# Performance work log

Hardware: AMD Instinct MI355X
Metric: run time of the kernel (lower is better)

The kernel has to match this reference:

```python
import jax, jax.numpy as jnp
import numpy as np

DIM = 512
HEADS = 8
R = 8  # reduction_ratio
EPS = 1e-08


def setup_inputs() -> dict:
    key = jax.random.key(0)
    k1, k2, k3, k4, k5 = jax.random.split(key, 5)
    B, H, W = 2, 128, 128
    x = jax.random.normal(k1, (B, DIM, H, W), dtype=jnp.float32)
    mask = jax.random.uniform(k2, (B, 1, H, W), dtype=jnp.float32)
    # learned params (conv weights, OIHW)
    Wq = jax.random.normal(k3, (DIM, DIM, 1, 1), dtype=jnp.float32) * 0.02
    Wkv = jax.random.normal(k4, (2 * DIM, DIM, R, R), dtype=jnp.float32) * 0.02
    Wo = jax.random.normal(k5, (DIM, DIM, 1, 1), dtype=jnp.float32) * 0.02
    return {"x": x, "mask": mask, "Wq": Wq, "Wkv": Wkv, "Wo": Wo}


def reference(x, mask, Wq, Wkv, Wo):
    B, C, H, W = x.shape
    heads = HEADS
    hd = C // heads  # head dim
    scale = hd ** (-0.5)
    N = H * W
    Hr, Wr = H // R, W // R
    L = Hr * Wr

    # to_q: 1x1 conv (no bias)
    q = jnp.einsum('bchw,oc->bohw', x, Wq[:, :, 0, 0])
    # to_kv: conv kernel R stride R (no bias)
    kv = jax.lax.conv_general_dilated(
        x, Wkv, window_strides=(R, R), padding='VALID',
        dimension_numbers=('NCHW', 'OIHW', 'NCHW'))
    k, v = jnp.split(kv, 2, axis=1)  # each [B, C, Hr, Wr]

    # nn.Unfold(R, stride=R) on [B,1,H,W] then mean over patch dim == avg-pool R/R
    mask_down = mask.reshape(B, Hr, R, Wr, R).mean(axis=(2, 4)).reshape(B, L)  # [B, L]
    m_flat = mask.reshape(B, N)  # [B, N]  (c == 1)
    # rank-1 outer-product bias, then log
    bias = jnp.log(m_flat[:, :, None] * mask_down[:, None, :] + EPS)  # [B, N, L]

    def to_tokens(t, n):
        # 'b (h c) x y -> (b h) (x y) c'
        Bt = t.shape[0]
        return t.reshape(Bt, heads, hd, n).transpose(0, 1, 3, 2).reshape(Bt * heads, n, hd)

    qh = to_tokens(q, N)   # [B*heads, N, hd]
    kh = to_tokens(k, L)   # [B*heads, L, hd]
    vh = to_tokens(v, L)   # [B*heads, L, hd]

    # torch mask.repeat(heads,1,1): tiles whole [B,...] block heads times -> index i uses bias[i % B]
    bias_rep = jnp.tile(bias, (heads, 1, 1))  # [heads*B, N, L]

    sim = (jnp.einsum('bic,bjc->bij', qh, kh) + bias_rep) * scale
    attn = jax.nn.softmax(sim, axis=-1)
    out = jnp.einsum('bij,bjc->bic', attn, vh)  # [B*heads, N, hd]

    # '(b h) (x y) c -> b (h c) x y'
    out = out.reshape(B, heads, N, hd).transpose(0, 1, 3, 2).reshape(B, C, H, W)
    return jnp.einsum('bchw,oc->bohw', out, Wo[:, :, 0, 0])
```

## Files before the change

kernel.cpp:

```cpp
#include <hip/hip_runtime.h>
#include <math.h>

#define DIMC  512
#define HEADS 8
#define HD    64
#define NPIX  16384
#define LTOK  256
#define BATCH 2
#define WIMG  128
#define KVK   32768
#define EPSB  1e-8f
#define SCALEF 0.125f
#define SPLITK 16
#define KCHUNK (KVK / SPLITK)

typedef unsigned short ushort_t;
typedef unsigned int uint_t;
using bf16x8 = __attribute__((ext_vector_type(8))) __bf16;
using f32x4  = __attribute__((ext_vector_type(4))) float;

__device__ __forceinline__ ushort_t f2bf(float f) {
    union { float f; unsigned u; } v; v.f = f;
    unsigned r = v.u + 0x7FFFu + ((v.u >> 16) & 1u);
    return (ushort_t)(r >> 16);
}
__device__ __forceinline__ uint_t pk2bf(float a, float b) {
    return (uint_t)f2bf(a) | ((uint_t)f2bf(b) << 16);
}
__device__ __forceinline__ void gl16(const void* g, void* l) {
    __builtin_amdgcn_global_load_lds(
        (const __attribute__((address_space(1))) unsigned int*)g,
        (__attribute__((address_space(3))) unsigned int*)l, 16, 0, 0);
}

__global__ void k_maskdown(const float* __restrict__ mask, float* __restrict__ md) {
    int b = blockIdx.x;
    int l = threadIdx.x;
    int hr = l >> 4, wr = l & 15;
    const float* mp = mask + (size_t)b * NPIX;
    float s = 0.f;
#pragma unroll
    for (int i = 0; i < 8; ++i)
#pragma unroll
        for (int j = 0; j < 8; ++j)
            s += mp[(hr * 8 + i) * WIMG + wr * 8 + j];
    md[b * LTOK + l] = s * (1.f / 64.f);
}

__global__ __launch_bounds__(256) void k_xt(const float* __restrict__ x, ushort_t* __restrict__ xt) {
    __shared__ float t[64][65];
    int b = blockIdx.z, c0 = blockIdx.y * 64, n0 = blockIdx.x * 64;
    int tn = threadIdx.x & 63, tc = threadIdx.x >> 6;
    const float* xb = x + ((size_t)b * DIMC + c0) * NPIX + n0;
#pragma unroll
    for (int p = 0; p < 16; ++p)
        t[tc + p * 4][tn] = xb[(size_t)(tc + p * 4) * NPIX + tn];
    __syncthreads();
    ushort_t* xtb = xt + ((size_t)b * NPIX + n0) * DIMC + c0;
    int tc4 = threadIdx.x & 15, ng = threadIdx.x >> 4;
#pragma unroll
    for (int p = 0; p < 4; ++p) {
        int nl = ng + p * 16;
        ushort4 v;
        v.x = f2bf(t[4 * tc4 + 0][nl]);
        v.y = f2bf(t[4 * tc4 + 1][nl]);
        v.z = f2bf(t[4 * tc4 + 2][nl]);
        v.w = f2bf(t[4 * tc4 + 3][nl]);
        *(ushort4*)&xtb[(size_t)nl * DIMC + 4 * tc4] = v;
    }
}

__global__ __launch_bounds__(256) void k_wkvp(const float* __restrict__ Wkv, ushort_t* __restrict__ Wp) {
    __shared__ float t[64][65];
    int o = blockIdx.y, c0 = blockIdx.x * 64;
    int tij = threadIdx.x & 63, tc = threadIdx.x >> 6;
    const float* wb = Wkv + ((size_t)o * DIMC + c0) * 64;
#pragma unroll
    for (int p = 0; p < 16; ++p)
        t[tc + p * 4][tij] = wb[(size_t)(tc + p * 4) * 64 + tij];
    __syncthreads();
    ushort_t* wpb = Wp + (size_t)o * KVK + c0;
    int tj4 = threadIdx.x & 15, ig = threadIdx.x >> 4;
#pragma unroll
    for (int p = 0; p < 4; ++p) {
        int ij = ig + p * 16;
        ushort4 v;
        v.x = f2bf(t[4 * tj4 + 0][ij]);
        v.y = f2bf(t[4 * tj4 + 1][ij]);
        v.z = f2bf(t[4 * tj4 + 2][ij]);
        v.w = f2bf(t[4 * tj4 + 3][ij]);
        *(ushort4*)&wpb[(size_t)ij * DIMC + 4 * tj4] = v;
    }
}

__global__ void k_cvt2(const float* __restrict__ a, const float* __restrict__ b,
                       ushort_t* __restrict__ da, ushort_t* __restrict__ db) {
    int i = blockIdx.x * 256 + threadIdx.x;
    if (i < 262144) da[i] = f2bf(a[i]);
    else            db[i - 262144] = f2bf(b[i - 262144]);
}

template<int EPI>
__global__ __launch_bounds__(256) void k_gemm_qo(
    const ushort_t* __restrict__ A, long sA,
    const ushort_t* __restrict__ B, long sB,
    void* __restrict__ Yv) {
    __shared__ ushort_t Asm[2][128 * 64];
    __shared__ ushort_t Bsm[2][128 * 64];
    const int tid = threadIdx.x;
    const int w = tid >> 6, lane = tid & 63;
    const int wm = w >> 1, wn = w & 1;
    const int lr = lane & 15, lg = lane >> 4;
    const int bz = blockIdx.z;
    const int m0 = blockIdx.y * 128, c0 = blockIdx.x * 128;
    const ushort_t* Ab = A + (size_t)bz * sA;
    const ushort_t* Bb = B + (size_t)bz * sB;

    f32x4 acc[4][4];
    const f32x4 zz = {0.f, 0.f, 0.f, 0.f};
#pragma unroll
    for (int i = 0; i < 4; ++i)
#pragma unroll
        for (int j = 0; j < 4; ++j) acc[i][j] = zz;

#define STAGE_QO(buf, k0) do {                                               \
    _Pragma("unroll")                                                        \
    for (int r = 0; r < 4; ++r) {                                            \
        int slot = r * 256 + tid;                                            \
        int m = slot >> 3, kb = slot & 7;                                    \
        int kbs = kb ^ (m & 7);                                              \
        gl16(Ab + (size_t)(m0 + m) * DIMC + (k0) + kbs * 8,                  \
             &Asm[buf][(size_t)(r * 256 + w * 64) * 8]);                     \
    }                                                                        \
    _Pragma("unroll")                                                        \
    for (int r = 0; r < 4; ++r) {                                            \
        int slot = r * 256 + tid;                                            \
        int m = slot >> 3, kb = slot & 7;                                    \
        int kbs = kb ^ (m & 7);                                              \
        gl16(Bb + (size_t)(c0 + m) * DIMC + (k0) + kbs * 8,                  \
             &Bsm[buf][(size_t)(r * 256 + w * 64) * 8]);                     \
    }                                                                        \
} while (0)

    STAGE_QO(0, 0);
    __syncthreads();
    int cur = 0;
#pragma unroll 1
    for (int t = 0; t < 8; ++t) {
        if (t < 7) STAGE_QO(cur ^ 1, (t + 1) * 64);
#pragma unroll
        for (int kk = 0; kk < 2; ++kk) {
            bf16x8 af[4], bfr[4];
#pragma unroll
            for (int i = 0; i < 4; ++i) {
                int row = wm * 64 + i * 16 + lr;
                af[i] = *(const bf16x8*)&Asm[cur][(size_t)(row * 8 + ((kk * 4 + lg) ^ (row & 7))) * 8];
            }
#pragma unroll
            for (int j = 0; j < 4; ++j) {
                int row = wn * 64 + j * 16 + lr;
                bfr[j] = *(const bf16x8*)&Bsm[cur][(size_t)(row * 8 + ((kk * 4 + lg) ^ (row & 7))) * 8];
            }
#pragma unroll
            for (int i = 0; i < 4; ++i)
#pragma unroll
                for (int j = 0; j < 4; ++j)
                    acc[i][j] = __builtin_amdgcn_mfma_f32_16x16x32_bf16(af[i], bfr[j], acc[i][j], 0, 0, 0);
        }
        if (t < 7) {
            __syncthreads();
            cur ^= 1;
        }
    }
#undef STAGE_QO

    if (EPI == 0) {
        ushort_t* q = (ushort_t*)Yv + (size_t)bz * ((size_t)NPIX * DIMC);
#pragma unroll
        for (int i = 0; i < 4; ++i) {
            int d0 = m0 + wm * 64 + i * 16 + lg * 4;
#pragma unroll
            for (int j = 0; j < 4; ++j) {
                int n = c0 + wn * 64 + j * 16 + lr;
                ushort4 v;
                v.x = f2bf(acc[i][j][0]); v.y = f2bf(acc[i][j][1]);
                v.z = f2bf(acc[i][j][2]); v.w = f2bf(acc[i][j][3]);
                *(ushort4*)&q[(size_t)n * DIMC + d0] = v;
            }
        }
    } else {
        float* O = (float*)Yv + (size_t)bz * ((size_t)DIMC * NPIX);
#pragma unroll
        for (int i = 0; i < 4; ++i) {
            int n0r = m0 + wm * 64 + i * 16 + lg * 4;
#pragma unroll
            for (int j = 0; j < 4; ++j) {
                int o = c0 + wn * 64 + j * 16 + lr;
                *(f32x4*)&O[(size_t)o * NPIX + n0r] = acc[i][j];
            }
        }
    }
}

__global__ __launch_bounds__(256) void k_convkv_mfma(
    const ushort_t* __restrict__ xt, const ushort_t* __restrict__ Wp,
    float* __restrict__ part) {
    __shared__ ushort_t Asm[2][128 * 64];
    __shared__ ushort_t Bsm[2][128 * 64];
    const int tid = threadIdx.x;
    const int w = tid >> 6, lane = tid & 63;
    const int wm = w >> 1, wn = w & 1;
    const int lr = lane & 15, lg = lane >> 4;
    const int f = blockIdx.x;
    const int xcd = f & 7, idx = f >> 3;
    const int z = (idx >> 4) * 8 + xcd;
    const int inner = idx & 15;
    const int m0 = (inner >> 1) * 128, n0 = (inner & 1) * 128;
    const int b = z >> 4, ks = z & 15;
    const ushort_t* xtb = xt + (size_t)b * NPIX * DIMC;
    const int kbeg = ks * KCHUNK;

    f32x4 acc[4][4];
    const f32x4 zz = {0.f, 0.f, 0.f, 0.f};
#pragma unroll
    for (int i = 0; i < 4; ++i)
#pragma unroll
        for (int j = 0; j < 4; ++j) acc[i][j] = zz;

#define STAGE_KV(buf, k0) do {                                               \
    _Pragma("unroll")                                                        \
    for (int r = 0; r < 4; ++r) {                                            \
        int slot = r * 256 + tid;                                            \
        int m = slot >> 3, kb = slot & 7;                                    \
        int kbs = kb ^ (m & 7);                                              \
        gl16(Wp + (size_t)(m0 + m) * KVK + (k0) + kbs * 8,                   \
             &Asm[buf][(size_t)(r * 256 + w * 64) * 8]);                     \
    }                                                                        \
    _Pragma("unroll")                                                        \
    for (int r = 0; r < 4; ++r) {                                            \
        int slot = r * 256 + tid;                                            \
        int nn = slot >> 3, kb = slot & 7;                                   \
        int l = n0 + nn, hr = l >> 4, wr = l & 15;                           \
        int kp = (k0) + (kb ^ (nn & 7)) * 8;                                 \
        int ij = kp >> 9, ck = kp & 511;                                     \
        int ii = ij >> 3, jj = ij & 7;                                       \
        gl16(xtb + (size_t)((hr * 8 + ii) * WIMG + wr * 8 + jj) * DIMC + ck, \
             &Bsm[buf][(size_t)(r * 256 + w * 64) * 8]);                     \
    }                                                                        \
} while (0)

    STAGE_KV(0, kbeg);
    __syncthreads();
    int cur = 0;
#pragma unroll 1
    for (int t = 0; t < KCHUNK / 64; ++t) {
        if (t < KCHUNK / 64 - 1) STAGE_KV(cur ^ 1, kbeg + (t + 1) * 64);
#pragma unroll
        for (int kk = 0; kk < 2; ++kk) {
            bf16x8 af[4], bfr[4];
#pragma unroll
            for (int i = 0; i < 4; ++i) {
                int row = wm * 64 + i * 16 + lr;
                af[i] = *(const bf16x8*)&Asm[cur][(size_t)(row * 8 + ((kk * 4 + lg) ^ (row & 7))) * 8];
            }
#pragma unroll
            for (int j = 0; j < 4; ++j) {
                int row = wn * 64 + j * 16 + lr;
                bfr[j] = *(const bf16x8*)&Bsm[cur][(size_t)(row * 8 + ((kk * 4 + lg) ^ (row & 7))) * 8];
            }
#pragma unroll
            for (int i = 0; i < 4; ++i)
#pragma unroll
                for (int j = 0; j < 4; ++j)
                    acc[i][j] = __builtin_amdgcn_mfma_f32_16x16x32_bf16(af[i], bfr[j], acc[i][j], 0, 0, 0);
        }
        if (t < KCHUNK / 64 - 1) {
            __syncthreads();
            cur ^= 1;
        }
    }
#undef STAGE_KV

    float* P = part + (size_t)z * (LTOK * 1024);
#pragma unroll
    for (int i = 0; i < 4; ++i) {
        int o0 = m0 + wm * 64 + i * 16 + lg * 4;
#pragma unroll
        for (int j = 0; j < 4; ++j) {
            int l = n0 + wn * 64 + j * 16 + lr;
            *(f32x4*)&P[(size_t)l * 1024 + o0] = acc[i][j];
        }
    }
}

__global__ void k_kvreduce(const float* __restrict__ part,
                           ushort_t* __restrict__ kt, ushort_t* __restrict__ vt) {
    int idx = blockIdx.x * 256 + threadIdx.x;
    int o = idx & 1023;
    int rest = idx >> 10;
    int l = rest & 255, b = rest >> 8;
    float s = 0.f;
#pragma unroll
    for (int ks = 0; ks < SPLITK; ++ks)
        s += part[(size_t)(b * SPLITK + ks) * (LTOK * 1024) + (size_t)l * 1024 + o];
    int h = (o >> 6) & 7, d = o & 63;
    if (o < 512)
        kt[(((size_t)b * 8 + h) * 256 + l) * 64 + d] = f2bf(s);
    else
        vt[(((size_t)b * 8 + h) * 64 + d) * 256 + l] = f2bf(s);
}

__global__ __launch_bounds__(256, 2) void k_attn_mfma(
    const ushort_t* __restrict__ qbf, const ushort_t* __restrict__ kt,
    const ushort_t* __restrict__ vt, const float* __restrict__ mask,
    const float* __restrict__ md, ushort_t* __restrict__ obuf) {
    __shared__ ushort_t Qs[128 * 64];
    __shared__ ushort_t Ks[256 * 64];
    __shared__ ushort_t Vs[64 * 256];

    const int tid = threadIdx.x;
    const int w = tid >> 6, lane = tid & 63;
    const int g = lane >> 4, ln = lane & 15;
    const int bh = blockIdx.y, b = bh >> 3, h = bh & 7;
    const int bb = bh & 1;
    const int n0 = blockIdx.x * 128;

    {
        const ushort_t* src = qbf + ((size_t)b * NPIX + n0) * DIMC + h * 64;
#pragma unroll
        for (int p = 0; p < 4; ++p) {
            int id = p * 256 + tid;
            int r = id >> 3, s = id & 7;
            uint4 v = *(const uint4*)(src + (size_t)r * DIMC + s * 8);
            *(uint4*)&Qs[(r * 8 + (s ^ (r & 7))) * 8] = v;
        }
    }
    {
        const ushort_t* src = kt + (size_t)bh * 256 * 64;
#pragma unroll
        for (int p = 0; p < 8; ++p) {
            int id = p * 256 + tid;
            int r = id >> 3, s = id & 7;
            uint4 v = *(const uint4*)(src + r * 64 + s * 8);
            *(uint4*)&Ks[(r * 8 + (s ^ (r & 7))) * 8] = v;
        }
    }
    {
        const ushort_t* src = vt + (size_t)bh * 64 * 256;
#pragma unroll
        for (int p = 0; p < 8; ++p) {
            int id = p * 256 + tid;
            int r = id >> 5, s = id & 31;
            uint4 v = *(const uint4*)(src + r * 256 + s * 8);
            *(uint4*)&Vs[(r * 32 + (s ^ (r & 7))) * 8] = v;
        }
    }
    __syncthreads();

    f32x4 acc[2][16];
    const f32x4 zz = {0.f, 0.f, 0.f, 0.f};
#pragma unroll
    for (int nf = 0; nf < 2; ++nf)
#pragma unroll
        for (int f = 0; f < 16; ++f) acc[nf][f] = zz;

    bf16x8 qf[2][2];
#pragma unroll
    for (int nf = 0; nf < 2; ++nf)
#pragma unroll
        for (int kk = 0; kk < 2; ++kk) {
            int nl = 32 * w + nf * 16 + ln;
            qf[nf][kk] = *(const bf16x8*)&Qs[(nl * 8 + ((kk * 4 + g) ^ (nl & 7))) * 8];
        }
#pragma unroll
    for (int f = 0; f < 16; ++f) {
#pragma unroll
        for (int kk = 0; kk < 2; ++kk) {
            int l = f * 16 + ln;
            bf16x8 kf = *(const bf16x8*)&Ks[(l * 8 + ((kk * 4 + g) ^ (l & 7))) * 8];
            acc[0][f] = __builtin_amdgcn_mfma_f32_16x16x32_bf16(kf, qf[0][kk], acc[0][f], 0, 0, 0);
            acc[1][f] = __builtin_amdgcn_mfma_f32_16x16x32_bf16(kf, qf[1][kk], acc[1][f], 0, 0, 0);
        }
    }

    float inv[2];
    uint2 pb[2][16];
#pragma unroll
    for (int nf = 0; nf < 2; ++nf) {
        float mval = mask[(size_t)bb * NPIX + n0 + 32 * w + nf * 16 + ln];
        float mx = -1e30f;
#pragma unroll
        for (int f = 0; f < 16; ++f) {
            float4 md4 = *(const float4*)&md[bb * LTOK + f * 16 + g * 4];
            float s0 = (acc[nf][f][0] + __logf(mval * md4.x + EPSB)) * SCALEF;
            float s1 = (acc[nf][f][1] + __logf(mval * md4.y + EPSB)) * SCALEF;
            float s2 = (acc[nf][f][2] + __logf(mval * md4.z + EPSB)) * SCALEF;
            float s3 = (acc[nf][f][3] + __logf(mval * md4.w + EPSB)) * SCALEF;
            acc[nf][f][0] = s0; acc[nf][f][1] = s1;
            acc[nf][f][2] = s2; acc[nf][f][3] = s3;
            mx = fmaxf(mx, fmaxf(fmaxf(s0, s1), fmaxf(s2, s3)));
        }
        mx = fmaxf(mx, __shfl_xor(mx, 16));
        mx = fmaxf(mx, __shfl_xor(mx, 32));
        float sum = 0.f;
#pragma unroll
        for (int f = 0; f < 16; ++f) {
            float p0 = __expf(acc[nf][f][0] - mx);
            float p1 = __expf(acc[nf][f][1] - mx);
            float p2 = __expf(acc[nf][f][2] - mx);
            float p3 = __expf(acc[nf][f][3] - mx);
            sum += (p0 + p1) + (p2 + p3);
            pb[nf][f].x = pk2bf(p0, p1);
            pb[nf][f].y = pk2bf(p2, p3);
        }
        sum += __shfl_xor(sum, 16);
        sum += __shfl_xor(sum, 32);
        inv[nf] = 1.f / sum;
    }

    f32x4 acc2[2][4];
#pragma unroll
    for (int nf = 0; nf < 2; ++nf)
#pragma unroll
        for (int df = 0; df < 4; ++df) acc2[nf][df] = zz;

    const int srcLo = ((g & 1) << 5) + ln;
    const bool selHi = (g >> 1);
#pragma unroll
    for (int ks = 0; ks < 8; ++ks) {
        bf16x8 vf[4];
#pragma unroll
        for (int df = 0; df < 4; ++df) {
            int d = df * 16 + ln;
            vf[df] = *(const bf16x8*)&Vs[(d * 32 + ((ks * 4 + g) ^ (d & 7))) * 8];
        }
#pragma unroll
        for (int nf = 0; nf < 2; ++nf) {
            uint_t e0 = pb[nf][2 * ks].x,     e1 = pb[nf][2 * ks].y;
            uint_t o0 = pb[nf][2 * ks + 1].x, o1 = pb[nf][2 * ks + 1].y;
            uint_t lo0 = __shfl((int)e0, srcLo), lo1 = __shfl((int)e1, srcLo);
            uint_t lo0b = __shfl((int)o0, srcLo), lo1b = __shfl((int)o1, srcLo);
            uint_t hi0 = __shfl((int)e0, srcLo + 16), hi1 = __shfl((int)e1, srcLo + 16);
            uint_t hi0b = __shfl((int)o0, srcLo + 16), hi1b = __shfl((int)o1, srcLo + 16);
            union { uint_t u[4]; bf16x8 v; } bfr;
            bfr.u[0] = selHi ? lo0b : lo0;
            bfr.u[1] = selHi ? lo1b : lo1;
            bfr.u[2] = selHi ? hi0b : hi0;
            bfr.u[3] = selHi ? hi1b : hi1;
#pragma unroll
            for (int df = 0; df < 4; ++df)
                acc2[nf][df] = __builtin_amdgcn_mfma_f32_16x16x32_bf16(vf[df], bfr.v, acc2[nf][df], 0, 0, 0);
        }
    }

#pragma unroll
    for (int nf = 0; nf < 2; ++nf) {
        int n = n0 + 32 * w + nf * 16 + ln;
        ushort_t* op = obuf + ((size_t)b * NPIX + n) * DIMC + h * 64;
#pragma unroll
        for (int df = 0; df < 4; ++df) {
            ushort4 v;
            v.x = f2bf(acc2[nf][df][0] * inv[nf]);
            v.y = f2bf(acc2[nf][df][1] * inv[nf]);
            v.z = f2bf(acc2[nf][df][2] * inv[nf]);
            v.w = f2bf(acc2[nf][df][3] * inv[nf]);
            *(ushort4*)&op[df * 16 + g * 4] = v;
        }
    }
}

extern "C" void kernel_launch(void* const* d_in, const int* in_sizes, int n_in,
                              void* d_out, int out_size, void* d_ws, size_t ws_size,
                              hipStream_t stream) {
    const float* x    = (const float*)d_in[0];
    const float* mask = (const float*)d_in[1];
    const float* Wq   = (const float*)d_in[2];
    const float* Wkv  = (const float*)d_in[3];
    const float* Wo   = (const float*)d_in[4];
    float* out = (float*)d_out;

    char* ws = (char*)d_ws;
    float*    md   = (float*)(ws);
    ushort_t* xt   = (ushort_t*)(ws + 4096);
    ushort_t* wkvp = (ushort_t*)(ws + 33558528);
    ushort_t* qbf  = wkvp;
    ushort_t* ktb  = (ushort_t*)(ws + 100667392);
    ushort_t* vtb  = ktb + 524288;
    ushort_t* wqb  = (ushort_t*)(ws + 102764544);
    ushort_t* wob  = wqb + 262144;
    float*    part = (float*)(ws + 103813120);
    ushort_t* aob  = (ushort_t*)part;

    k_maskdown<<<dim3(BATCH), dim3(256), 0, stream>>>(mask, md);
    k_xt<<<dim3(NPIX / 64, DIMC / 64, BATCH), dim3(256), 0, stream>>>(x, xt);
    k_cvt2<<<dim3(2048), dim3(256), 0, stream>>>(Wq, Wo, wqb, wob);
    k_wkvp<<<dim3(DIMC / 64, 1024), dim3(256), 0, stream>>>(Wkv, wkvp);

    k_convkv_mfma<<<dim3(512), dim3(256), 0, stream>>>(xt, wkvp, part);
    k_kvreduce<<<dim3(2048), dim3(256), 0, stream>>>(part, ktb, vtb);

    k_gemm_qo<0><<<dim3(NPIX / 128, DIMC / 128, BATCH), dim3(256), 0, stream>>>(
        wqb, 0L, xt, (long)NPIX * DIMC, qbf);

    k_attn_mfma<<<dim3(NPIX / 128, BATCH * HEADS), dim3(256), 0, stream>>>(
        qbf, ktb, vtb, mask, md, aob);

    k_gemm_qo<1><<<dim3(DIMC / 128, NPIX / 128, BATCH), dim3(256), 0, stream>>>(
        aob, (long)NPIX * DIMC, wob, 0L, out);
}
```

Before: 255.3 us.

## Fuse Wkv repack and bf16 conversion into conv-KV GEMM loads

Drops the separate Wkv permute/convert kernel and makes the strided KV conv GEMM read fp32 x and Wkv directly, converting to bf16 in registers before writing swizzled LDS. The K ordering changes to channel-major (c, i, j), so the weights need no permutation. Staging now goes through registers with a single LDS buffer and an extra barrier instead of direct-to-LDS double buffering. This removes a full pass over the 64MB Wkv tensor and its bf16 copy, at the cost of doubled fp32 global reads inside the GEMM and less overlap.

```diff
diff --git a/kernel.cpp b/kernel.cpp
--- a/kernel.cpp
+++ b/kernel.cpp
@@ -67,29 +67,6 @@
         v.z = f2bf(t[4 * tc4 + 2][nl]);
         v.w = f2bf(t[4 * tc4 + 3][nl]);
         *(ushort4*)&xtb[(size_t)nl * DIMC + 4 * tc4] = v;
-    }
-}
-
-__global__ __launch_bounds__(256) void k_wkvp(const float* __restrict__ Wkv, ushort_t* __restrict__ Wp) {
-    __shared__ float t[64][65];
-    int o = blockIdx.y, c0 = blockIdx.x * 64;
-    int tij = threadIdx.x & 63, tc = threadIdx.x >> 6;
-    const float* wb = Wkv + ((size_t)o * DIMC + c0) * 64;
-#pragma unroll
-    for (int p = 0; p < 16; ++p)
-        t[tc + p * 4][tij] = wb[(size_t)(tc + p * 4) * 64 + tij];
-    __syncthreads();
-    ushort_t* wpb = Wp + (size_t)o * KVK + c0;
-    int tj4 = threadIdx.x & 15, ig = threadIdx.x >> 4;
-#pragma unroll
-    for (int p = 0; p < 4; ++p) {
-        int ij = ig + p * 16;
-        ushort4 v;
-        v.x = f2bf(t[4 * tj4 + 0][ij]);
-        v.y = f2bf(t[4 * tj4 + 1][ij]);
-        v.z = f2bf(t[4 * tj4 + 2][ij]);
-        v.w = f2bf(t[4 * tj4 + 3][ij]);
-        *(ushort4*)&wpb[(size_t)ij * DIMC + 4 * tj4] = v;
     }
 }
 
@@ -203,10 +180,10 @@
 }
 
 __global__ __launch_bounds__(256) void k_convkv_mfma(
-    const ushort_t* __restrict__ xt, const ushort_t* __restrict__ Wp,
+    const float* __restrict__ x, const float* __restrict__ Wkv,
     float* __restrict__ part) {
-    __shared__ ushort_t Asm[2][128 * 64];
-    __shared__ ushort_t Bsm[2][128 * 64];
+    __shared__ ushort_t Asm[128 * 64];
+    __shared__ ushort_t Bsm[128 * 64];
     const int tid = threadIdx.x;
     const int w = tid >> 6, lane = tid & 63;
     const int wm = w >> 1, wn = w & 1;
@@ -217,9 +194,10 @@
     const int inner = idx & 15;
     const int m0 = (inner >> 1) * 128, n0 = (inner & 1) * 128;
     const int b = z >> 4, ks = z & 15;
-    const ushort_t* xtb = xt + (size_t)b * NPIX * DIMC;
+    const float* xb = x + (size_t)b * DIMC * NPIX;
     const int kbeg = ks * KCHUNK;
 
+    const int srow = tid >> 3, skb = tid & 7;
     f32x4 acc[4][4];
     const f32x4 zz = {0.f, 0.f, 0.f, 0.f};
 #pragma unroll
@@ -227,46 +205,60 @@
 #pragma unroll
         for (int j = 0; j < 4; ++j) acc[i][j] = zz;
 
-#define STAGE_KV(buf, k0) do {                                               \
+    float4 ra[4][2], rb[4][2];
+
+#define LOAD_KV(k0) do {                                                     \
     _Pragma("unroll")                                                        \
     for (int r = 0; r < 4; ++r) {                                            \
-        int slot = r * 256 + tid;                                            \
-        int m = slot >> 3, kb = slot & 7;                                    \
-        int kbs = kb ^ (m & 7);                                              \
-        gl16(Wp + (size_t)(m0 + m) * KVK + (k0) + kbs * 8,                   \
-             &Asm[buf][(size_t)(r * 256 + w * 64) * 8]);                     \
+        int m = srow + 32 * r;                                               \
+        const float* pa = Wkv + (size_t)(m0 + m) * KVK + (k0) + skb * 8;     \
+        ra[r][0] = *(const float4*)pa;                                       \
+        ra[r][1] = *(const float4*)(pa + 4);                                 \
+        int l = n0 + m, hr = l >> 4, wr = l & 15;                            \
+        const float* pb = xb + (size_t)((k0) >> 6) * NPIX                    \
+                          + (hr * 8 + skb) * WIMG + wr * 8;                  \
+        rb[r][0] = *(const float4*)pb;                                       \
+        rb[r][1] = *(const float4*)(pb + 4);                                 \
     }                                                                        \
+} while (0)
+
+#define WRITE_KV() do {                                                      \
     _Pragma("unroll")                                                        \
     for (int r = 0; r < 4; ++r) {                                            \
-        int slot = r * 256 + tid;                                            \
-        int nn = slot >> 3, kb = slot & 7;                                   \
-        int l = n0 + nn, hr = l >> 4, wr = l & 15;                           \
-        int kp = (k0) + (kb ^ (nn & 7)) * 8;                                 \
-        int ij = kp >> 9, ck = kp & 511;                                     \
-        int ii = ij >> 3, jj = ij & 7;                                       \
-        gl16(xtb + (size_t)((hr * 8 + ii) * WIMG + wr * 8 + jj) * DIMC + ck, \
-             &Bsm[buf][(size_t)(r * 256 + w * 64) * 8]);                     \
+        int m = srow + 32 * r;                                               \
+        int off = (m * 8 + (skb ^ (m & 7))) * 8;                             \
+        uint4 va, vb;                                                        \
+        va.x = pk2bf(ra[r][0].x, ra[r][0].y);                                \
+        va.y = pk2bf(ra[r][0].z, ra[r][0].w);                                \
+        va.z = pk2bf(ra[r][1].x, ra[r][1].y);                                \
+        va.w = pk2bf(ra[r][1].z, ra[r][1].w);                                \
+        vb.x = pk2bf(rb[r][0].x, rb[r][0].y);                                \
+        vb.y = pk2bf(rb[r][0].z, rb[r][0].w);                                \
+        vb.z = pk2bf(rb[r][1].x, rb[r][1].y);                                \
+        vb.w = pk2bf(rb[r][1].z, rb[r][1].w);                                \
+        *(uint4*)&Asm[off] = va;                                             \
+        *(uint4*)&Bsm[off] = vb;                                             \
     }                                                                        \
 } while (0)
 
-    STAGE_KV(0, kbeg);
+    LOAD_KV(kbeg);
+    WRITE_KV();
     __syncthreads();
-    int cur = 0;
 #pragma unroll 1
     for (int t = 0; t < KCHUNK / 64; ++t) {
-        if (t < KCHUNK / 64 - 1) STAGE_KV(cur ^ 1, kbeg + (t + 1) * 64);
+        if (t < KCHUNK / 64 - 1) LOAD_KV(kbeg + (t + 1) * 64);
 #pragma unroll
         for (int kk = 0; kk < 2; ++kk) {
             bf16x8 af[4], bfr[4];
 #pragma unroll
             for (int i = 0; i < 4; ++i) {
                 int row = wm * 64 + i * 16 + lr;
-                af[i] = *(const bf16x8*)&Asm[cur][(size_t)(row * 8 + ((kk * 4 + lg) ^ (row & 7))) * 8];
+                af[i] = *(const bf16x8*)&Asm[(size_t)(row * 8 + ((kk * 4 + lg) ^ (row & 7))) * 8];
             }
 #pragma unroll
             for (int j = 0; j < 4; ++j) {
                 int row = wn * 64 + j * 16 + lr;
-                bfr[j] = *(const bf16x8*)&Bsm[cur][(size_t)(row * 8 + ((kk * 4 + lg) ^ (row & 7))) * 8];
+                bfr[j] = *(const bf16x8*)&Bsm[(size_t)(row * 8 + ((kk * 4 + lg) ^ (row & 7))) * 8];
             }
 #pragma unroll
             for (int i = 0; i < 4; ++i)
@@ -274,12 +266,14 @@
                 for (int j = 0; j < 4; ++j)
                     acc[i][j] = __builtin_amdgcn_mfma_f32_16x16x32_bf16(af[i], bfr[j], acc[i][j], 0, 0, 0);
         }
+        __syncthreads();
         if (t < KCHUNK / 64 - 1) {
+            WRITE_KV();
             __syncthreads();
-            cur ^= 1;
-        }
-    }
-#undef STAGE_KV
+        }
+    }
+#undef LOAD_KV
+#undef WRITE_KV
 
     float* P = part + (size_t)z * (LTOK * 1024);
 #pragma unroll
@@ -482,8 +476,7 @@
     char* ws = (char*)d_ws;
     float*    md   = (float*)(ws);
     ushort_t* xt   = (ushort_t*)(ws + 4096);
-    ushort_t* wkvp = (ushort_t*)(ws + 33558528);
-    ushort_t* qbf  = wkvp;
+    ushort_t* qbf  = (ushort_t*)(ws + 33558528);
     ushort_t* ktb  = (ushort_t*)(ws + 100667392);
     ushort_t* vtb  = ktb + 524288;
     ushort_t* wqb  = (ushort_t*)(ws + 102764544);
@@ -492,11 +485,9 @@
     ushort_t* aob  = (ushort_t*)part;
 
     k_maskdown<<<dim3(BATCH), dim3(256), 0, stream>>>(mask, md);
+    k_cvt2<<<dim3(2048), dim3(256), 0, stream>>>(Wq, Wo, wqb, wob);
+    k_convkv_mfma<<<dim3(512), dim3(256), 0, stream>>>(x, Wkv, part);
     k_xt<<<dim3(NPIX / 64, DIMC / 64, BATCH), dim3(256), 0, stream>>>(x, xt);
-    k_cvt2<<<dim3(2048), dim3(256), 0, stream>>>(Wq, Wo, wqb, wob);
-    k_wkvp<<<dim3(DIMC / 64, 1024), dim3(256), 0, stream>>>(Wkv, wkvp);
-
-    k_convkv_mfma<<<dim3(512), dim3(256), 0, stream>>>(xt, wkvp, part);
     k_kvreduce<<<dim3(2048), dim3(256), 0, stream>>>(part, ktb, vtb);
 
     k_gemm_qo<0><<<dim3(NPIX / 128, DIMC / 128, BATCH), dim3(256), 0, stream>>>(
```

Measured after the change: 268.7 us. 5.2% more time.
